# Performance work log

Hardware: AMD Instinct MI355X
Metric: run time of the kernel (lower is better)

## Reference

```python
import jax, jax.numpy as jnp
import numpy as np

T = 8
TAU = 0.25
THRESH = 0.5

# --- constants derived from T, tau (match torch __init__) ---
_idx = jnp.arange(T)
_powers = jnp.clip(_idx[:, None] - _idx[None, :], 0)
W_CONST = jnp.tril(TAU * (1.0 - TAU) ** _powers).astype(jnp.float32)           # [T,T]
COEFF = jnp.tril(TAU ** (_idx[:, None] - _idx[None, :]).astype(jnp.float32))   # [T,T] tril(tau^(i-j))
IG, JG = jnp.meshgrid(_idx, _idx, indexing='ij')
MASK = (((IG > JG) & (JG <= IG - 2)) | (IG == JG + 1)).astype(jnp.float32)     # [T,T]


def setup_inputs() -> dict:
    key = jax.random.key(0)
    x = jax.random.normal(key, (T, 128, 16384), dtype=jnp.float32)
    return {"x": x}


def reference(x):
    x_flat = x.reshape(T, -1)                                   # [T, dim]
    dim = x_flat.shape[1]
    # membrane-potential survival probability per step
    p1 = jax.nn.sigmoid(THRESH - 0.5 * (TAU * x_flat + W_CONST @ x_flat))
    # log-domain cumulative products, prepended with zeros row
    log_cumsum = jnp.concatenate(
        [jnp.zeros((1, dim), x.dtype),
         jnp.cumsum(jnp.log(jnp.maximum(p1, 1e-12)), axis=0)], axis=0)  # [T+1, dim]
    # pairwise log ratios; masked-out entries -> 0 -> exp = 1 (as in torch code)
    log_ratio = log_cumsum[IG] - log_cumsum[JG]                  # [T, T, dim]
    reset1 = jnp.exp(log_ratio * MASK[:, :, None])               # [T, T, dim]
    pre = jnp.einsum('ijc,jc->ic', TAU * reset1 * COEFF[:, :, None], x_flat) - THRESH
    s = (pre > 0).astype(x.dtype)                                 # surrogate forward = heaviside
    return s.reshape(x.shape)
```

## Files before the change

kernel.cpp:

```cpp
#include <hip/hip_runtime.h>
#include <cmath>


#define TT 8

typedef float vfloat4 __attribute__((ext_vector_type(4)));

#define STEP32(xik, w, S, o)                                  \
    {                                                         \
        float xk_ = (xik);                                    \
        w = fmaf(0.75f, w, 0.25f * xk_);                      \
        float arg_ = fmaf(-0.5f, fmaf(0.25f, xk_, w), 0.5f);  \
        float t_ = __expf(-arg_);                             \
        float p1_ = __builtin_amdgcn_rcpf(1.0f + t_);         \
        float sx_ = S + xk_;                                  \
        float pre_ = fmaf(0.25f, sx_, -0.5f);                 \
        o = (pre_ > 0.0f) ? 1.0f : 0.0f;                      \
        float a_ = fabsf(pre_);                               \
        mn = (a_ < mn) ? a_ : mn;                             \
        S = 0.25f * p1_ * sx_;                                \
    }

#define STEP64(xif, wd, Sd, o)                                \
    {                                                         \
        double xd_ = (double)(xif);                           \
        wd = 0.25 * xd_ + 0.75 * wd;                          \
        double arg_ = 0.5 - 0.5 * (0.25 * xd_ + wd);          \
        double p1_ = 1.0 / (1.0 + exp(-arg_));                \
        double pre_ = 0.25 * (xd_ + Sd) - 0.5;                \
        o = (pre_ > 0.0) ? 1.0f : 0.0f;                       \
        Sd = 0.25 * p1_ * (Sd + xd_);                         \
    }

__global__ __launch_bounds__(256)
void pa_lif_kernel(const float* __restrict__ x, float* __restrict__ out, int dim4) {
    int tid = blockIdx.x * blockDim.x + threadIdx.x;
    if (tid >= dim4) return;

    const float4* __restrict__ xv = (const float4*)x;
    float4* __restrict__ ov = (float4*)out;
    vfloat4* __restrict__ onv = (vfloat4*)out;

    float4 xr[TT];
#pragma unroll
    for (int i = 0; i < TT; ++i)
        xr[i] = xv[(size_t)i * dim4 + tid];

    float4 ot[TT];
    float w0 = 0.f, w1 = 0.f, w2 = 0.f, w3 = 0.f;
    float S0 = 0.f, S1 = 0.f, S2 = 0.f, S3 = 0.f;
    float mn = 1e30f;

#pragma unroll
    for (int i = 0; i < TT; ++i) {
        STEP32(xr[i].x, w0, S0, ot[i].x);
        STEP32(xr[i].y, w1, S1, ot[i].y);
        STEP32(xr[i].z, w2, S2, ot[i].z);
        STEP32(xr[i].w, w3, S3, ot[i].w);
    }

    if (__builtin_expect(mn >= 5e-5f, 1)) {
#pragma unroll
        for (int i = 0; i < TT; ++i) {
            vfloat4 o = {ot[i].x, ot[i].y, ot[i].z, ot[i].w};
            __builtin_nontemporal_store(o, &onv[(size_t)i * dim4 + tid]);
        }
    } else {
        double wd0 = 0, wd1 = 0, wd2 = 0, wd3 = 0;
        double Sd0 = 0, Sd1 = 0, Sd2 = 0, Sd3 = 0;
#pragma unroll
        for (int i = 0; i < TT; ++i) {
            float4 xi = xr[i];
            float4 o;
            STEP64(xi.x, wd0, Sd0, o.x);
            STEP64(xi.y, wd1, Sd1, o.y);
            STEP64(xi.z, wd2, Sd2, o.z);
            STEP64(xi.w, wd3, Sd3, o.w);
            ov[(size_t)i * dim4 + tid] = o;
        }
    }
}

extern "C" void kernel_launch(void* const* d_in, const int* in_sizes, int n_in,
                              void* d_out, int out_size, void* d_ws, size_t ws_size,
                              hipStream_t stream) {
    (void)n_in; (void)out_size; (void)d_ws; (void)ws_size;
    const float* x = (const float*)d_in[0];
    float* out = (float*)d_out;
    int total = in_sizes[0];
    int dim = total / TT;
    int dim4 = dim / 4;
    int block = 256;
    int grid = (dim4 + block - 1) / block;
    pa_lif_kernel<<<grid, block, 0, stream>>>(x, out, dim4);
}
```

Measured before the change: 110.4 us.

## Defer rare double-precision refinement to a separate compacted kernel

The fast kernel now stores fp32 results right away inside the time loop, so it no longer holds all eight output vectors in registers. Threads whose decision margin is too small push their index onto a workspace list with a wave-aggregated atomic. A second kernel then recomputes only those elements in double precision. This takes the divergent fp64 path out of the main kernel and lowers register pressure, at the cost of an extra memset, an extra launch, and writing some outputs twice.

```diff
diff --git a/kernel.cpp b/kernel.cpp
--- a/kernel.cpp
+++ b/kernel.cpp
@@ -3,6 +3,7 @@
 
 
 #define TT 8
+#define REFINE_THRESH 5e-5f
 
 typedef float vfloat4 __attribute__((ext_vector_type(4)));
 
@@ -33,7 +34,8 @@
     }
 
 __global__ __launch_bounds__(256)
-void pa_lif_kernel(const float* __restrict__ x, float* __restrict__ out, int dim4) {
+void pa_lif_fast(const float* __restrict__ x, float* __restrict__ out, int dim4,
+                 unsigned* __restrict__ ws, unsigned capacity) {
     int tid = blockIdx.x * blockDim.x + threadIdx.x;
     if (tid >= dim4) return;
 
@@ -46,31 +48,79 @@
     for (int i = 0; i < TT; ++i)
         xr[i] = xv[(size_t)i * dim4 + tid];
 
-    float4 ot[TT];
     float w0 = 0.f, w1 = 0.f, w2 = 0.f, w3 = 0.f;
     float S0 = 0.f, S1 = 0.f, S2 = 0.f, S3 = 0.f;
     float mn = 1e30f;
 
 #pragma unroll
     for (int i = 0; i < TT; ++i) {
-        STEP32(xr[i].x, w0, S0, ot[i].x);
-        STEP32(xr[i].y, w1, S1, ot[i].y);
-        STEP32(xr[i].z, w2, S2, ot[i].z);
-        STEP32(xr[i].w, w3, S3, ot[i].w);
+        vfloat4 o;
+        STEP32(xr[i].x, w0, S0, o.x);
+        STEP32(xr[i].y, w1, S1, o.y);
+        STEP32(xr[i].z, w2, S2, o.z);
+        STEP32(xr[i].w, w3, S3, o.w);
+        __builtin_nontemporal_store(o, &onv[(size_t)i * dim4 + tid]);
     }
 
-    if (__builtin_expect(mn >= 5e-5f, 1)) {
-#pragma unroll
-        for (int i = 0; i < TT; ++i) {
-            vfloat4 o = {ot[i].x, ot[i].y, ot[i].z, ot[i].w};
-            __builtin_nontemporal_store(o, &onv[(size_t)i * dim4 + tid]);
+    bool need = (mn < REFINE_THRESH);
+    unsigned long long mask = __ballot(need);
+    if (need) {
+        int lane = threadIdx.x & 63;
+        int myidx = __popcll(mask & ((1ULL << lane) - 1ULL));
+        if (capacity != 0u) {
+            unsigned base = 0;
+            if (myidx == 0)
+                base = atomicAdd(ws, (unsigned)__popcll(mask));
+            base = __builtin_amdgcn_readfirstlane(base);
+            unsigned slot = base + (unsigned)myidx;
+            if (slot < capacity) {
+                ws[4 + slot] = (unsigned)tid;
+            } else {
+                double wd0 = 0, wd1 = 0, wd2 = 0, wd3 = 0;
+                double Sd0 = 0, Sd1 = 0, Sd2 = 0, Sd3 = 0;
+#pragma unroll 1
+                for (int i = 0; i < TT; ++i) {
+                    float4 xi = xv[(size_t)i * dim4 + tid];
+                    float4 o;
+                    STEP64(xi.x, wd0, Sd0, o.x);
+                    STEP64(xi.y, wd1, Sd1, o.y);
+                    STEP64(xi.z, wd2, Sd2, o.z);
+                    STEP64(xi.w, wd3, Sd3, o.w);
+                    ov[(size_t)i * dim4 + tid] = o;
+                }
+            }
+        } else {
+            double wd0 = 0, wd1 = 0, wd2 = 0, wd3 = 0;
+            double Sd0 = 0, Sd1 = 0, Sd2 = 0, Sd3 = 0;
+#pragma unroll 1
+            for (int i = 0; i < TT; ++i) {
+                float4 xi = xv[(size_t)i * dim4 + tid];
+                float4 o;
+                STEP64(xi.x, wd0, Sd0, o.x);
+                STEP64(xi.y, wd1, Sd1, o.y);
+                STEP64(xi.z, wd2, Sd2, o.z);
+                STEP64(xi.w, wd3, Sd3, o.w);
+                ov[(size_t)i * dim4 + tid] = o;
+            }
         }
-    } else {
+    }
+}
+
+__global__ __launch_bounds__(256)
+void pa_lif_refine(const float* __restrict__ x, float* __restrict__ out, int dim4,
+                   const unsigned* __restrict__ ws, unsigned capacity) {
+    unsigned count = ws[0];
+    if (count > capacity) count = capacity;
+    const float4* __restrict__ xv = (const float4*)x;
+    float4* __restrict__ ov = (float4*)out;
+    unsigned stride = gridDim.x * blockDim.x;
+    for (unsigned k = blockIdx.x * blockDim.x + threadIdx.x; k < count; k += stride) {
+        int tid = (int)ws[4 + k];
         double wd0 = 0, wd1 = 0, wd2 = 0, wd3 = 0;
         double Sd0 = 0, Sd1 = 0, Sd2 = 0, Sd3 = 0;
-#pragma unroll
+#pragma unroll 1
         for (int i = 0; i < TT; ++i) {
-            float4 xi = xr[i];
+            float4 xi = xv[(size_t)i * dim4 + tid];
             float4 o;
             STEP64(xi.x, wd0, Sd0, o.x);
             STEP64(xi.y, wd1, Sd1, o.y);
@@ -84,7 +134,7 @@
 extern "C" void kernel_launch(void* const* d_in, const int* in_sizes, int n_in,
                               void* d_out, int out_size, void* d_ws, size_t ws_size,
                               hipStream_t stream) {
-    (void)n_in; (void)out_size; (void)d_ws; (void)ws_size;
+    (void)n_in; (void)out_size;
     const float* x = (const float*)d_in[0];
     float* out = (float*)d_out;
     int total = in_sizes[0];
@@ -92,5 +142,20 @@
     int dim4 = dim / 4;
     int block = 256;
     int grid = (dim4 + block - 1) / block;
-    pa_lif_kernel<<<grid, block, 0, stream>>>(x, out, dim4);
+
+    unsigned capacity = 0;
+    unsigned* ws = (unsigned*)d_ws;
+    if (ws != nullptr && ws_size >= 32) {
+        size_t cap = (ws_size - 16) / 4;
+        if (cap > (size_t)dim4) cap = (size_t)dim4;
+        capacity = (unsigned)cap;
+    }
+
+    if (capacity != 0u) {
+        hipMemsetAsync(d_ws, 0, 16, stream);
+        pa_lif_fast<<<grid, block, 0, stream>>>(x, out, dim4, ws, capacity);
+        pa_lif_refine<<<256, block, 0, stream>>>(x, out, dim4, ws, capacity);
+    } else {
+        pa_lif_fast<<<grid, block, 0, stream>>>(x, out, dim4, ws, 0u);
+    }
 }
```

Result: slower. 115.5 us (+4.7%).
